# Kernel optimization log

Measured on AMD Instinct MI355X. Metric: run time of the kernel, lower is better.

## Reference

```python
import jax, jax.numpy as jnp
import numpy as np

B = 65536      # batch size
XD = 64        # x_dim: number of DAG nodes / tabular features
HD = 128       # h_dim
F_SCALE = 0.1  # f_scale weight shrink applied after xavier init


def _xavier(key, shape, fan_in, fan_out, scale):
    std = float(np.sqrt(2.0 / (fan_in + fan_out)))
    return jax.random.normal(key, shape, jnp.float32) * (std * scale)


def setup_inputs() -> dict:
    key = jax.random.key(0)
    ks = jax.random.split(key, 8)
    x = jax.random.uniform(ks[0], (B, XD), jnp.float32)
    z = jax.random.normal(ks[1], (B, XD, 1), jnp.float32)  # noise regenerated inside torch forward
    # learnable soft adjacency M: rand*0.2 with zero diagonal (dag_seed == [])
    M = jax.random.uniform(ks[2], (XD, XD), jnp.float32) * 0.2
    M = M * (1.0 - jnp.eye(XD, dtype=jnp.float32))
    # per-node input layers fc_i[i]: Linear(XD+1, HD), xavier*f_scale, column i zeroed (1e-16)
    Wi = _xavier(ks[3], (XD, HD, XD + 1), XD + 1, HD, F_SCALE)
    idx = jnp.arange(XD)
    Wi = Wi.at[idx, :, idx].set(1e-16)
    bi = jnp.zeros((XD, HD), jnp.float32)
    # shared MLP: Linear(HD,HD)+ReLU twice, xavier*f_scale
    Ws1 = _xavier(ks[4], (HD, HD), HD, HD, F_SCALE)
    bs1 = jnp.zeros((HD,), jnp.float32)
    Ws2 = _xavier(ks[5], (HD, HD), HD, HD, F_SCALE)
    bs2 = jnp.zeros((HD,), jnp.float32)
    # per-node output heads fc_f[i]: Linear(HD, 1), xavier*f_scale
    wf = _xavier(ks[6], (XD, HD), HD, 1, F_SCALE)
    bf = jnp.zeros((XD,), jnp.float32)
    return {"x": x, "z": z, "M": M, "Wi": Wi, "bi": bi, "Ws1": Ws1,
            "bs1": bs1, "Ws2": Ws2, "bs2": bs2, "wf": wf, "bf": bf}


def reference(x, z, M, Wi, bi, Ws1, bs1, Ws2, bs2, wf, bf):
    # Generator_causal.sequential with choice='original', gen_order=range(XD), biased_edges={}
    zT = jnp.transpose(z, (1, 0, 2))  # [XD, B, 1], z[:, i, :] per step
    Mcols = M.T                       # row i == M[:, i] (parent mask of node i)
    idx = jnp.arange(XD)

    def step(out, xs):
        i, mcol, Wi_i, bi_i, wf_i, bf_i, z_i = xs
        xm = out * mcol                         # adjacency-masked parent gather [B, XD]
        xm = xm.at[:, i].set(0.0)               # x_masked[:, i] = 0
        h = jnp.concatenate([xm, z_i], axis=1)  # [B, XD+1]
        h = jax.nn.relu(h @ Wi_i.T + bi_i)      # fc_i[i] + ReLU
        h = jax.nn.relu(h @ Ws1.T + bs1)        # shared block 1
        h = jax.nn.relu(h @ Ws2.T + bs2)        # shared block 2
        o = jax.nn.sigmoid(h @ wf_i + bf_i)     # fc_f[i] -> [B]
        out = out.at[:, i].set(o)               # scatter write into out[:, i]
        return out, None

    out, _ = jax.lax.scan(step, x, (idx, Mcols, Wi, bi, wf, bf, zT))
    return out
```

## Files before the change

kernel.cpp:

```cpp
#include <hip/hip_runtime.h>

#define XD 64
#define HD 128
#define RB 64
#define NT 256
#define BLOB 18432
#define N_STEP_CHUNKS 18

#define OFF_STEP0 0
#define OFF_STEP1 18432
#define OFF_H1    36864
#define OFF_H2    53248
#define OFF_OUT   69632
#define OFF_ZC    77824
#define OFF_BS1   78336
#define OFF_BS2   78848
#define OFF_PART  79360
#define SMEM_BYTES 80384

typedef __attribute__((ext_vector_type(8))) short short8;
typedef __attribute__((ext_vector_type(4))) float f32x4;
typedef __attribute__((ext_vector_type(2))) unsigned int u32x2;
typedef unsigned int u32;

__device__ __forceinline__ short f2bf(float f) {
    union { float f; unsigned u; } v; v.f = f;
    unsigned r = (v.u + 0x7FFFu + ((v.u >> 16) & 1u)) >> 16;
    return (short)r;
}
__device__ __forceinline__ float bf2f(short s) {
    union { float f; unsigned u; } v;
    v.u = ((unsigned)(unsigned short)s) << 16;
    return v.f;
}
__device__ __forceinline__ u32 cvtpk2(float a, float b) {
    u32 r;
    asm("v_cvt_pk_bf16_f32 %0, %1, %2" : "=v"(r) : "v"(a), "v"(b));
    return r;
}

__device__ __forceinline__ void* swz128(char* base, int row, int byteoff) {
    return base + row * 128 + (byteoff ^ ((row & 7) << 4));
}
__device__ __forceinline__ void* swz256(char* base, int row, int byteoff) {
    return base + row * 256 + (byteoff ^ ((row & 7) << 4));
}

__device__ __forceinline__ void gload16(const void* g, void* l) {
    __builtin_amdgcn_global_load_lds(
        (const __attribute__((address_space(1))) u32*)g,
        (__attribute__((address_space(3))) u32*)l, 16, 0, 0);
}

__global__ void prep_kernel(const float* __restrict__ Wi, const float* __restrict__ M,
                            const float* __restrict__ bi, const float* __restrict__ wf,
                            const float* __restrict__ bf, char* __restrict__ ws)
{
    int idx = blockIdx.x * 256 + threadIdx.x;
    if (idx < XD * HD * 8) {
        int i  = idx >> 10;
        int n  = (idx >> 3) & 127;
        int kc = idx & 7;
        const float* src = Wi + ((size_t)i * HD + n) * (XD + 1) + kc * 8;
        short8 v;
        #pragma unroll
        for (int j = 0; j < 8; ++j) {
            int k = kc * 8 + j;
            float m = (k == i) ? 0.0f : M[k * XD + i];
            v[j] = f2bf(src[j] * m);
        }
        char* dst = ws + (size_t)i * BLOB + n * 128 + ((kc * 16) ^ ((n & 7) << 4));
        *(short8*)dst = v;
    } else {
        int r = idx - XD * HD * 8;
        if (r < XD * HD) {
            int i = r >> 7, n = r & 127;
            float* d = (float*)(ws + (size_t)i * BLOB + 16384);
            d[n]       = Wi[((size_t)i * HD + n) * (XD + 1) + XD];
            d[128 + n] = bi[i * HD + n];
            d[256 + n] = wf[i * HD + n];
            if (n == 0) d[384] = bf[i];
        }
    }
}

__global__ __launch_bounds__(NT, 2) void gen_kernel(
    const float* __restrict__ x,   const float* __restrict__ z,
    const float* __restrict__ Ws1, const float* __restrict__ Ws2,
    const float* __restrict__ bs1, const float* __restrict__ bs2,
    const char*  __restrict__ blob, float* __restrict__ out)
{
    extern __shared__ char smem[];
    const int tid  = threadIdx.x;
    const int row0 = blockIdx.x * RB;
    const int wave = tid >> 6, lane = tid & 63;
    const int lg = lane >> 4, lc = lane & 15;
    const int wn = wave;

    char*  sH1  = smem + OFF_H1;
    char*  sH2  = smem + OFF_H2;
    char*  sOUT = smem + OFF_OUT;
    float* sZC  = (float*)(smem + OFF_ZC);
    float* sBS1 = (float*)(smem + OFF_BS1);
    float* sBS2 = (float*)(smem + OFF_BS2);
    float* sPART= (float*)(smem + OFF_PART);

    for (int c = wave; c < N_STEP_CHUNKS; c += 4)
        gload16(blob + c * 1024 + lane * 16, smem + OFF_STEP0 + c * 1024);
    if (tid < RB)
        sZC[tid] = z[(size_t)(row0 + tid) * XD + 0];
    for (int c = tid; c < RB * 8; c += NT) {
        int r = c >> 3, kc = c & 7;
        const float* xs = x + (size_t)(row0 + r) * XD + kc * 8;
        short8 v;
        #pragma unroll
        for (int j = 0; j < 8; ++j) v[j] = f2bf(xs[j]);
        *(short8*)swz128(sOUT, r, kc * 16) = v;
    }
    if (tid < HD) { sBS1[tid] = bs1[tid]; sBS2[tid] = bs2[tid]; }

    short8 BW1[2][4], BW2[2][4];
    #pragma unroll
    for (int t = 0; t < 2; ++t) {
        int n = wn * 32 + t * 16 + lc;
        #pragma unroll
        for (int s = 0; s < 4; ++s) {
            const float* p1 = Ws1 + n * HD + s * 32 + lg * 8;
            const float* p2 = Ws2 + n * HD + s * 32 + lg * 8;
            #pragma unroll
            for (int j = 0; j < 8; ++j) {
                BW1[t][s][j] = f2bf(p1[j]);
                BW2[t][s][j] = f2bf(p2[j]);
            }
        }
    }
    __syncthreads();

    float zreg = 0.f;
    for (int i = 0; i < XD; ++i) {
        char* sWIb = smem + ((i & 1) ? OFF_STEP1 : OFF_STEP0);
        char* sWIn = smem + ((i & 1) ? OFF_STEP0 : OFF_STEP1);
        const float* blobS = (const float*)(sWIb + 16384);
        float* zcur = sZC + (i & 1) * RB;
        float* znxt = sZC + ((i + 1) & 1) * RB;

        if (i + 1 < XD) {
            const char* gb = blob + (size_t)(i + 1) * BLOB;
            for (int c = wave; c < N_STEP_CHUNKS; c += 4)
                gload16(gb + c * 1024 + lane * 16, sWIn + c * 1024);
            if (tid < RB) zreg = z[(size_t)(row0 + tid) * XD + (i + 1)];
        }

        short8 aW[2][2];
        #pragma unroll
        for (int t = 0; t < 2; ++t) {
            int n = wn * 32 + t * 16 + lc;
            aW[t][0] = *(const short8*)swz128(sWIb, n, lg * 16);
            aW[t][1] = *(const short8*)swz128(sWIb, n, 64 + lg * 16);
        }
        #pragma unroll
        for (int m = 0; m < 4; ++m) {
            int r = m * 16 + lc;
            short8 b0 = *(const short8*)swz128(sOUT, r, lg * 16);
            short8 b1 = *(const short8*)swz128(sOUT, r, 64 + lg * 16);
            float zm = zcur[r];
            #pragma unroll
            for (int t = 0; t < 2; ++t) {
                int nb = wn * 32 + t * 16;
                f32x4 wiz = *(const f32x4*)&blobS[nb + lg * 4];
                f32x4 c   = *(const f32x4*)&blobS[128 + nb + lg * 4];
                c = __builtin_amdgcn_mfma_f32_16x16x32_bf16(aW[t][0], b0, c, 0, 0, 0);
                c = __builtin_amdgcn_mfma_f32_16x16x32_bf16(aW[t][1], b1, c, 0, 0, 0);
                float v0 = fmaxf(c[0] + zm * wiz[0], 0.f);
                float v1 = fmaxf(c[1] + zm * wiz[1], 0.f);
                float v2 = fmaxf(c[2] + zm * wiz[2], 0.f);
                float v3 = fmaxf(c[3] + zm * wiz[3], 0.f);
                u32x2 w = { cvtpk2(v0, v1), cvtpk2(v2, v3) };
                *(u32x2*)swz256(sH1, r, 2 * nb + lg * 8) = w;
            }
        }
        __syncthreads();

        #pragma unroll
        for (int m = 0; m < 4; ++m) {
            int r = m * 16 + lc;
            short8 bH[4];
            #pragma unroll
            for (int s = 0; s < 4; ++s)
                bH[s] = *(const short8*)swz256(sH1, r, s * 64 + lg * 16);
            #pragma unroll
            for (int t = 0; t < 2; ++t) {
                int nb = wn * 32 + t * 16;
                f32x4 c = *(const f32x4*)&sBS1[nb + lg * 4];
                #pragma unroll
                for (int s = 0; s < 4; ++s)
                    c = __builtin_amdgcn_mfma_f32_16x16x32_bf16(BW1[t][s], bH[s], c, 0, 0, 0);
                u32x2 w = { cvtpk2(fmaxf(c[0], 0.f), fmaxf(c[1], 0.f)),
                            cvtpk2(fmaxf(c[2], 0.f), fmaxf(c[3], 0.f)) };
                *(u32x2*)swz256(sH2, r, 2 * nb + lg * 8) = w;
            }
        }
        __syncthreads();

        #pragma unroll
        for (int m = 0; m < 4; ++m) {
            int r = m * 16 + lc;
            short8 bH[4];
            #pragma unroll
            for (int s = 0; s < 4; ++s)
                bH[s] = *(const short8*)swz256(sH2, r, s * 64 + lg * 16);
            float op = 0.f;
            #pragma unroll
            for (int t = 0; t < 2; ++t) {
                int nb = wn * 32 + t * 16;
                f32x4 c = *(const f32x4*)&sBS2[nb + lg * 4];
                #pragma unroll
                for (int s = 0; s < 4; ++s)
                    c = __builtin_amdgcn_mfma_f32_16x16x32_bf16(BW2[t][s], bH[s], c, 0, 0, 0);
                f32x4 wf4 = *(const f32x4*)&blobS[256 + nb + lg * 4];
                op += fmaxf(c[0], 0.f) * wf4[0];
                op += fmaxf(c[1], 0.f) * wf4[1];
                op += fmaxf(c[2], 0.f) * wf4[2];
                op += fmaxf(c[3], 0.f) * wf4[3];
            }
            op += __shfl_xor(op, 16, 64);
            op += __shfl_xor(op, 32, 64);
            if (lg == 0) sPART[wn * RB + r] = op;
        }
        __syncthreads();

        if (tid < RB) {
            float p = sPART[tid] + sPART[RB + tid] + sPART[2*RB + tid] + sPART[3*RB + tid]
                      + blobS[384];
            float o = 1.0f / (1.0f + __expf(-p));
            *(short*)swz128(sOUT, tid, 2 * i) = f2bf(o);
            if (i + 1 < XD) znxt[tid] = zreg;
        }
        __syncthreads();
    }

    for (int c = tid; c < RB * 8; c += NT) {
        int r = c >> 3, kc = c & 7;
        short8 v = *(const short8*)swz128(sOUT, r, kc * 16);
        float* o = out + (size_t)(row0 + r) * XD + kc * 8;
        #pragma unroll
        for (int j = 0; j < 8; ++j) o[j] = bf2f(v[j]);
    }
}

extern "C" void kernel_launch(void* const* d_in, const int* in_sizes, int n_in,
                              void* d_out, int out_size, void* d_ws, size_t ws_size,
                              hipStream_t stream) {
    const float* x   = (const float*)d_in[0];
    const float* z   = (const float*)d_in[1];
    const float* M   = (const float*)d_in[2];
    const float* Wi  = (const float*)d_in[3];
    const float* bi  = (const float*)d_in[4];
    const float* Ws1 = (const float*)d_in[5];
    const float* bs1 = (const float*)d_in[6];
    const float* Ws2 = (const float*)d_in[7];
    const float* bs2 = (const float*)d_in[8];
    const float* wf  = (const float*)d_in[9];
    const float* bf  = (const float*)d_in[10];
    float* outp = (float*)d_out;
    char*  ws   = (char*)d_ws;

    prep_kernel<<<288, 256, 0, stream>>>(Wi, M, bi, wf, bf, ws);

    hipFuncSetAttribute(reinterpret_cast<const void*>(gen_kernel),
                        hipFuncAttributeMaxDynamicSharedMemorySize, SMEM_BYTES);
    gen_kernel<<<65536 / RB, NT, SMEM_BYTES, stream>>>(
        x, z, Ws1, Ws2, bs1, bs2, ws, outp);
}
```

Before: 550.1 us.

## Halve block rows and threads, single-buffer step weights, custom barriers

Shrinks each block to 32 rows and 2 waves, with each wave covering 64 hidden outputs. The per-step weight blob now sits in one LDS buffer, and the next step's load is issued after the first barrier instead of being double-buffered. LDS use roughly halves so more blocks fit per CU, and the custom barriers wait only on LDS counters except at the end of each step. The costs are more register pressure from the larger BW1/BW2 arrays and a prefetch window that now covers only the later phases of each step.

```diff
diff --git a/kernel.cpp b/kernel.cpp
--- a/kernel.cpp
+++ b/kernel.cpp
@@ -2,21 +2,20 @@
 
 #define XD 64
 #define HD 128
-#define RB 64
-#define NT 256
+#define RB 32
+#define NT 128
 #define BLOB 18432
 #define N_STEP_CHUNKS 18
 
-#define OFF_STEP0 0
-#define OFF_STEP1 18432
-#define OFF_H1    36864
-#define OFF_H2    53248
-#define OFF_OUT   69632
-#define OFF_ZC    77824
-#define OFF_BS1   78336
-#define OFF_BS2   78848
-#define OFF_PART  79360
-#define SMEM_BYTES 80384
+#define OFF_STEP 0
+#define OFF_H1   18432
+#define OFF_H2   26624
+#define OFF_OUT  34816
+#define OFF_ZC   38912
+#define OFF_BS1  39168
+#define OFF_BS2  39680
+#define OFF_PART 40192
+#define SMEM_BYTES 40448
 
 typedef __attribute__((ext_vector_type(8))) short short8;
 typedef __attribute__((ext_vector_type(4))) float f32x4;
@@ -37,6 +36,13 @@
     u32 r;
     asm("v_cvt_pk_bf16_f32 %0, %1, %2" : "=v"(r) : "v"(a), "v"(b));
     return r;
+}
+
+__device__ __forceinline__ void bar_lgkm() {
+    asm volatile("s_waitcnt lgkmcnt(0)\n\ts_barrier" ::: "memory");
+}
+__device__ __forceinline__ void bar_full() {
+    asm volatile("s_waitcnt vmcnt(0) lgkmcnt(0)\n\ts_barrier" ::: "memory");
 }
 
 __device__ __forceinline__ void* swz128(char* base, int row, int byteoff) {
@@ -97,6 +103,7 @@
     const int lg = lane >> 4, lc = lane & 15;
     const int wn = wave;
 
+    char*  sWI  = smem + OFF_STEP;
     char*  sH1  = smem + OFF_H1;
     char*  sH2  = smem + OFF_H2;
     char*  sOUT = smem + OFF_OUT;
@@ -104,9 +111,10 @@
     float* sBS1 = (float*)(smem + OFF_BS1);
     float* sBS2 = (float*)(smem + OFF_BS2);
     float* sPART= (float*)(smem + OFF_PART);
-
-    for (int c = wave; c < N_STEP_CHUNKS; c += 4)
-        gload16(blob + c * 1024 + lane * 16, smem + OFF_STEP0 + c * 1024);
+    const float* blobS = (const float*)(sWI + 16384);
+
+    for (int c = wave; c < N_STEP_CHUNKS; c += 2)
+        gload16(blob + c * 1024 + lane * 16, sWI + c * 1024);
     if (tid < RB)
         sZC[tid] = z[(size_t)(row0 + tid) * XD + 0];
     for (int c = tid; c < RB * 8; c += NT) {
@@ -117,12 +125,12 @@
         for (int j = 0; j < 8; ++j) v[j] = f2bf(xs[j]);
         *(short8*)swz128(sOUT, r, kc * 16) = v;
     }
-    if (tid < HD) { sBS1[tid] = bs1[tid]; sBS2[tid] = bs2[tid]; }
-
-    short8 BW1[2][4], BW2[2][4];
+    sBS1[tid] = bs1[tid];  sBS2[tid] = bs2[tid];
+
+    short8 BW1[4][4], BW2[4][4];
     #pragma unroll
-    for (int t = 0; t < 2; ++t) {
-        int n = wn * 32 + t * 16 + lc;
+    for (int t = 0; t < 4; ++t) {
+        int n = wn * 64 + t * 16 + lc;
         #pragma unroll
         for (int s = 0; s < 4; ++s) {
             const float* p1 = Ws1 + n * HD + s * 32 + lg * 8;
@@ -138,35 +146,31 @@
 
     float zreg = 0.f;
     for (int i = 0; i < XD; ++i) {
-        char* sWIb = smem + ((i & 1) ? OFF_STEP1 : OFF_STEP0);
-        char* sWIn = smem + ((i & 1) ? OFF_STEP0 : OFF_STEP1);
-        const float* blobS = (const float*)(sWIb + 16384);
         float* zcur = sZC + (i & 1) * RB;
         float* znxt = sZC + ((i + 1) & 1) * RB;
 
-        if (i + 1 < XD) {
-            const char* gb = blob + (size_t)(i + 1) * BLOB;
-            for (int c = wave; c < N_STEP_CHUNKS; c += 4)
-                gload16(gb + c * 1024 + lane * 16, sWIn + c * 1024);
-            if (tid < RB) zreg = z[(size_t)(row0 + tid) * XD + (i + 1)];
-        }
-
-        short8 aW[2][2];
-        #pragma unroll
-        for (int t = 0; t < 2; ++t) {
-            int n = wn * 32 + t * 16 + lc;
-            aW[t][0] = *(const short8*)swz128(sWIb, n, lg * 16);
-            aW[t][1] = *(const short8*)swz128(sWIb, n, 64 + lg * 16);
-        }
-        #pragma unroll
-        for (int m = 0; m < 4; ++m) {
+        f32x4 wfr[4];
+        #pragma unroll
+        for (int t = 0; t < 4; ++t)
+            wfr[t] = *(const f32x4*)&blobS[256 + wn * 64 + t * 16 + lg * 4];
+        float bfr = blobS[384];
+
+        short8 aW[4][2];
+        #pragma unroll
+        for (int t = 0; t < 4; ++t) {
+            int n = wn * 64 + t * 16 + lc;
+            aW[t][0] = *(const short8*)swz128(sWI, n, lg * 16);
+            aW[t][1] = *(const short8*)swz128(sWI, n, 64 + lg * 16);
+        }
+        #pragma unroll
+        for (int m = 0; m < 2; ++m) {
             int r = m * 16 + lc;
             short8 b0 = *(const short8*)swz128(sOUT, r, lg * 16);
             short8 b1 = *(const short8*)swz128(sOUT, r, 64 + lg * 16);
             float zm = zcur[r];
             #pragma unroll
-            for (int t = 0; t < 2; ++t) {
-                int nb = wn * 32 + t * 16;
+            for (int t = 0; t < 4; ++t) {
+                int nb = wn * 64 + t * 16;
                 f32x4 wiz = *(const f32x4*)&blobS[nb + lg * 4];
                 f32x4 c   = *(const f32x4*)&blobS[128 + nb + lg * 4];
                 c = __builtin_amdgcn_mfma_f32_16x16x32_bf16(aW[t][0], b0, c, 0, 0, 0);
@@ -179,18 +183,25 @@
                 *(u32x2*)swz256(sH1, r, 2 * nb + lg * 8) = w;
             }
         }
-        __syncthreads();
-
-        #pragma unroll
-        for (int m = 0; m < 4; ++m) {
+        bar_lgkm();
+
+        if (i + 1 < XD) {
+            const char* gb = blob + (size_t)(i + 1) * BLOB;
+            for (int c = wave; c < N_STEP_CHUNKS; c += 2)
+                gload16(gb + c * 1024 + lane * 16, sWI + c * 1024);
+            if (tid < RB) zreg = z[(size_t)(row0 + tid) * XD + (i + 1)];
+        }
+
+        #pragma unroll
+        for (int m = 0; m < 2; ++m) {
             int r = m * 16 + lc;
             short8 bH[4];
             #pragma unroll
             for (int s = 0; s < 4; ++s)
                 bH[s] = *(const short8*)swz256(sH1, r, s * 64 + lg * 16);
             #pragma unroll
-            for (int t = 0; t < 2; ++t) {
-                int nb = wn * 32 + t * 16;
+            for (int t = 0; t < 4; ++t) {
+                int nb = wn * 64 + t * 16;
                 f32x4 c = *(const f32x4*)&sBS1[nb + lg * 4];
                 #pragma unroll
                 for (int s = 0; s < 4; ++s)
@@ -200,10 +211,10 @@
                 *(u32x2*)swz256(sH2, r, 2 * nb + lg * 8) = w;
             }
         }
-        __syncthreads();
-
-        #pragma unroll
-        for (int m = 0; m < 4; ++m) {
+        bar_lgkm();
+
+        #pragma unroll
+        for (int m = 0; m < 2; ++m) {
             int r = m * 16 + lc;
             short8 bH[4];
             #pragma unroll
@@ -211,32 +222,29 @@
                 bH[s] = *(const short8*)swz256(sH2, r, s * 64 + lg * 16);
             float op = 0.f;
             #pragma unroll
-            for (int t = 0; t < 2; ++t) {
-                int nb = wn * 32 + t * 16;
-                f32x4 c = *(const f32x4*)&sBS2[nb + lg * 4];
+            for (int t = 0; t < 4; ++t) {
+                f32x4 c = *(const f32x4*)&sBS2[wn * 64 + t * 16 + lg * 4];
                 #pragma unroll
                 for (int s = 0; s < 4; ++s)
                     c = __builtin_amdgcn_mfma_f32_16x16x32_bf16(BW2[t][s], bH[s], c, 0, 0, 0);
-                f32x4 wf4 = *(const f32x4*)&blobS[256 + nb + lg * 4];
-                op += fmaxf(c[0], 0.f) * wf4[0];
-                op += fmaxf(c[1], 0.f) * wf4[1];
-                op += fmaxf(c[2], 0.f) * wf4[2];
-                op += fmaxf(c[3], 0.f) * wf4[3];
+                op += fmaxf(c[0], 0.f) * wfr[t][0];
+                op += fmaxf(c[1], 0.f) * wfr[t][1];
+                op += fmaxf(c[2], 0.f) * wfr[t][2];
+                op += fmaxf(c[3], 0.f) * wfr[t][3];
             }
             op += __shfl_xor(op, 16, 64);
             op += __shfl_xor(op, 32, 64);
             if (lg == 0) sPART[wn * RB + r] = op;
         }
-        __syncthreads();
+        bar_lgkm();
 
         if (tid < RB) {
-            float p = sPART[tid] + sPART[RB + tid] + sPART[2*RB + tid] + sPART[3*RB + tid]
-                      + blobS[384];
+            float p = sPART[tid] + sPART[RB + tid] + bfr;
             float o = 1.0f / (1.0f + __expf(-p));
             *(short*)swz128(sOUT, tid, 2 * i) = f2bf(o);
             if (i + 1 < XD) znxt[tid] = zreg;
         }
-        __syncthreads();
+        bar_full();
     }
 
     for (int c = tid; c < RB * 8; c += NT) {
```

Measured after the change: 575.0 us. 4.5% more time.
